# Kernel tuning notes

Hardware: AMD Instinct MI355X
Metric: run time of the kernel (lower is better)

## Reference

```python
import jax, jax.numpy as jnp
import numpy as np
import math

D_MODEL, D_STATE, SEQ_L = 1024, 64, 2048

def setup_inputs() -> dict:
    key = jax.random.key(0)
    k_dt, k_C = jax.random.split(key, 2)
    log_dt = jax.random.uniform(k_dt, (D_MODEL,), minval=math.log(0.001), maxval=math.log(0.1)).astype(jnp.float32)
    A_real = -0.5 * jnp.ones((D_MODEL, D_STATE), dtype=jnp.float32)
    A_imag = (jnp.repeat(jnp.arange(D_STATE, dtype=jnp.float32)[None, :], D_MODEL, axis=0) * math.pi)
    C = (jax.random.normal(k_C, (D_MODEL, D_STATE, 2)) * 0.5).astype(jnp.float32)
    return {"log_dt": log_dt, "A_real": A_real, "A_imag": A_imag, "C": C, "L": SEQ_L}

def reference(log_dt, A_real, A_imag, C, L):
    # dt: (D,1); A, C: (D,N) complex
    dt = jnp.exp(log_dt)[:, None]
    A = jax.lax.complex(A_real, A_imag)
    Cc = jax.lax.complex(C[..., 0], C[..., 1])
    dt_A = A * dt                                   # (D, N)
    A_bar = (1 + dt_A / 2) / (1 - dt_A / 2)         # (D, N) bilinear discretization
    B_bar = dt / (1 - dt_A / 2)                     # (D, N)
    z_inv = jnp.exp(-2j * jnp.pi * jnp.arange(L) / L)  # (L,) unit-circle frequencies
    # Cauchy-style broadcast-reduce: sum_n (C*B)_n / (1 - A_bar_n * z_inv_l)
    num = (Cc * B_bar)[:, :, None]                  # (D, N, 1)
    denom = 1 - A_bar[:, :, None] * z_inv[None, None, :]  # (D, N, L)
    H_z = jnp.sum(num / denom, axis=1)              # (D, L) complex transfer function
    return H_z
```

## Files before the change

kernel.cpp:

```cpp
#include <hip/hip_runtime.h>
#include <math.h>

constexpr int D_MODEL = 1024;
constexpr int D_STATE = 64;
constexpr int SEQ_L   = 2048;
constexpr int BLOCK   = 256;
constexpr int IPT     = 8;

__global__ __launch_bounds__(BLOCK) void s4_cauchy_real_kernel(
    const float* __restrict__ log_dt,
    const float* __restrict__ A_real,
    const float* __restrict__ A_imag,
    const float* __restrict__ C,
    float* __restrict__ out)
{
    __shared__ float s_abr[D_STATE];
    __shared__ float s_abi[D_STATE];
    __shared__ float s_nr [D_STATE];
    __shared__ float s_ni [D_STATE];

    const int d   = blockIdx.x;
    const int tid = threadIdx.x;

    if (tid < D_STATE) {
        const int n = tid;
        const float dt = __expf(log_dt[d]);
        const float ar = A_real[d * D_STATE + n];
        const float ai = A_imag[d * D_STATE + n];
        const float xr = 0.5f * dt * ar;
        const float xi = 0.5f * dt * ai;
        const float dr = 1.0f - xr;
        const float di = -xi;
        const float inv = 1.0f / (dr * dr + di * di);
        const float pr = 1.0f + xr;
        const float pi = xi;
        const float abr = (pr * dr + pi * di) * inv;
        const float abi = (pi * dr - pr * di) * inv;
        const float bbr =  dt * dr * inv;
        const float bbi = -dt * di * inv;
        const float cr = C[(d * D_STATE + n) * 2 + 0];
        const float ci = C[(d * D_STATE + n) * 2 + 1];
        s_abr[n] = abr;
        s_abi[n] = abi;
        s_nr[n]  = cr * bbr - ci * bbi;
        s_ni[n]  = cr * bbi + ci * bbr;
    }
    __syncthreads();

    float zr[IPT], zi[IPT], acc[IPT];
#pragma unroll
    for (int k = 0; k < IPT; ++k) {
        const int l = tid + k * BLOCK;
        const float theta = (2.0f * 3.14159265358979323846f * (float)l) / (float)SEQ_L;
        float s, c;
        __sincosf(theta, &s, &c);
        zr[k] = c;
        zi[k] = -s;
        acc[k] = 0.0f;
    }

#pragma unroll 4
    for (int n = 0; n < D_STATE; ++n) {
        const float abr = s_abr[n];
        const float abi = s_abi[n];
        const float nr  = s_nr[n];
        const float ni  = s_ni[n];
#pragma unroll
        for (int k = 0; k < IPT; ++k) {
            const float dr  = fmaf(-abr, zr[k], fmaf(abi, zi[k], 1.0f));
            const float di  = fmaf(-abr, zi[k], (-abi) * zr[k]);
            const float mag = fmaf(di, di, dr * dr);
            const float num = fmaf(ni, di, nr * dr);
            acc[k] = fmaf(num, __builtin_amdgcn_rcpf(mag), acc[k]);
        }
    }

#pragma unroll
    for (int k = 0; k < IPT; ++k)
        out[d * SEQ_L + tid + k * BLOCK] = acc[k];
}

__global__ __launch_bounds__(BLOCK) void s4_cauchy_complex_kernel(
    const float* __restrict__ log_dt, const float* __restrict__ A_real,
    const float* __restrict__ A_imag, const float* __restrict__ C,
    float* __restrict__ out)
{
    __shared__ float s_abr[D_STATE], s_abi[D_STATE], s_nr[D_STATE], s_ni[D_STATE];
    const int d    = blockIdx.x / (SEQ_L / BLOCK);
    const int lblk = blockIdx.x % (SEQ_L / BLOCK);
    const int tid  = threadIdx.x;
    if (tid < D_STATE) {
        const int n = tid;
        const float dt = __expf(log_dt[d]);
        const float ar = A_real[d * D_STATE + n], ai = A_imag[d * D_STATE + n];
        const float xr = 0.5f * dt * ar, xi = 0.5f * dt * ai;
        const float dr = 1.0f - xr, di = -xi;
        const float inv = 1.0f / (dr * dr + di * di);
        const float pr = 1.0f + xr, pi = xi;
        s_abr[n] = (pr * dr + pi * di) * inv;
        s_abi[n] = (pi * dr - pr * di) * inv;
        const float bbr = dt * dr * inv, bbi = -dt * di * inv;
        const float cr = C[(d * D_STATE + n) * 2 + 0], ci = C[(d * D_STATE + n) * 2 + 1];
        s_nr[n] = cr * bbr - ci * bbi;
        s_ni[n] = cr * bbi + ci * bbr;
    }
    __syncthreads();
    const int l = lblk * BLOCK + tid;
    const float theta = (2.0f * 3.14159265358979323846f * (float)l) / (float)SEQ_L;
    float s, c; __sincosf(theta, &s, &c);
    const float zr = c, zi = -s;
    float accr = 0.f, acci = 0.f;
#pragma unroll
    for (int n = 0; n < D_STATE; ++n) {
        const float abr = s_abr[n], abi = s_abi[n], nr = s_nr[n], ni = s_ni[n];
        const float dr = 1.0f - (abr * zr - abi * zi);
        const float di = -(abr * zi + abi * zr);
        const float inv = __builtin_amdgcn_rcpf(dr * dr + di * di);
        accr += (nr * dr + ni * di) * inv;
        acci += (ni * dr - nr * di) * inv;
    }
    float2* o = reinterpret_cast<float2*>(out);
    o[d * SEQ_L + l] = make_float2(accr, acci);
}

extern "C" void kernel_launch(void* const* d_in, const int* in_sizes, int n_in,
                              void* d_out, int out_size, void* d_ws, size_t ws_size,
                              hipStream_t stream) {
    const float* log_dt = (const float*)d_in[0];
    const float* A_real = (const float*)d_in[1];
    const float* A_imag = (const float*)d_in[2];
    const float* C      = (const float*)d_in[3];
    float* out = (float*)d_out;

    if (out_size >= 2 * D_MODEL * SEQ_L) {
        dim3 grid(D_MODEL * (SEQ_L / BLOCK));
        s4_cauchy_complex_kernel<<<grid, dim3(BLOCK), 0, stream>>>(log_dt, A_real, A_imag, C, out);
    } else {
        dim3 grid(D_MODEL);
        s4_cauchy_real_kernel<<<grid, dim3(BLOCK), 0, stream>>>(log_dt, A_real, A_imag, C, out);
    }
}
```

Measured before the change: 33.78 us.

## Pack real Cauchy kernel with f32x2 math, antipodal symmetry, and shared reciprocal

Rewrites the real-output kernel to use packed two-wide float vectors so the compiler can emit packed FMA instructions. It uses the z(l+L/2) = -z(l) symmetry to compute the A_bar*z product once for two output points. It also merges the two reciprocals into one rcp of the product of the two magnitudes. This cuts ALU and transcendental work per state element, at the cost of possible overflow or precision loss in mag1*mag2 and doubled shared-memory storage of broadcast coefficients.

```diff
diff --git a/kernel.cpp b/kernel.cpp
--- a/kernel.cpp
+++ b/kernel.cpp
@@ -5,7 +5,12 @@
 constexpr int D_STATE = 64;
 constexpr int SEQ_L   = 2048;
 constexpr int BLOCK   = 256;
-constexpr int IPT     = 8;
+
+typedef float f32x2 __attribute__((ext_vector_type(2)));
+
+static __device__ __forceinline__ f32x2 fma2(f32x2 a, f32x2 b, f32x2 c) {
+    return __builtin_elementwise_fma(a, b, c);
+}
 
 __global__ __launch_bounds__(BLOCK) void s4_cauchy_real_kernel(
     const float* __restrict__ log_dt,
@@ -14,10 +19,10 @@
     const float* __restrict__ C,
     float* __restrict__ out)
 {
-    __shared__ float s_abr[D_STATE];
-    __shared__ float s_abi[D_STATE];
-    __shared__ float s_nr [D_STATE];
-    __shared__ float s_ni [D_STATE];
+    __shared__ f32x2 s_ab_r[D_STATE];
+    __shared__ f32x2 s_ab_i[D_STATE];
+    __shared__ f32x2 s_n_r [D_STATE];
+    __shared__ f32x2 s_n_i [D_STATE];
 
     const int d   = blockIdx.x;
     const int tid = threadIdx.x;
@@ -40,44 +45,65 @@
         const float bbi = -dt * di * inv;
         const float cr = C[(d * D_STATE + n) * 2 + 0];
         const float ci = C[(d * D_STATE + n) * 2 + 1];
-        s_abr[n] = abr;
-        s_abi[n] = abi;
-        s_nr[n]  = cr * bbr - ci * bbi;
-        s_ni[n]  = cr * bbi + ci * bbr;
+        const float nr = cr * bbr - ci * bbi;
+        const float ni = cr * bbi + ci * bbr;
+        s_ab_r[n] = (f32x2){abr, abr};
+        s_ab_i[n] = (f32x2){abi, abi};
+        s_n_r [n] = (f32x2){nr, nr};
+        s_n_i [n] = (f32x2){ni, ni};
     }
     __syncthreads();
 
-    float zr[IPT], zi[IPT], acc[IPT];
+    f32x2 zr2[2], zi2[2], acc2[4];
 #pragma unroll
-    for (int k = 0; k < IPT; ++k) {
-        const int l = tid + k * BLOCK;
-        const float theta = (2.0f * 3.14159265358979323846f * (float)l) / (float)SEQ_L;
-        float s, c;
-        __sincosf(theta, &s, &c);
-        zr[k] = c;
-        zi[k] = -s;
-        acc[k] = 0.0f;
+    for (int kp = 0; kp < 2; ++kp) {
+#pragma unroll
+        for (int j = 0; j < 2; ++j) {
+            const int l = tid + (2 * kp + j) * BLOCK;
+            const float theta = (2.0f * 3.14159265358979323846f * (float)l) / (float)SEQ_L;
+            float s, c;
+            __sincosf(theta, &s, &c);
+            zr2[kp][j] = c;
+            zi2[kp][j] = -s;
+        }
+        acc2[kp]     = (f32x2){0.0f, 0.0f};
+        acc2[kp + 2] = (f32x2){0.0f, 0.0f};
     }
 
-#pragma unroll 4
+#pragma unroll 2
     for (int n = 0; n < D_STATE; ++n) {
-        const float abr = s_abr[n];
-        const float abi = s_abi[n];
-        const float nr  = s_nr[n];
-        const float ni  = s_ni[n];
+        const f32x2 ab_r = s_ab_r[n];
+        const f32x2 ab_i = s_ab_i[n];
+        const f32x2 n_r  = s_n_r[n];
+        const f32x2 n_i  = s_n_i[n];
 #pragma unroll
-        for (int k = 0; k < IPT; ++k) {
-            const float dr  = fmaf(-abr, zr[k], fmaf(abi, zi[k], 1.0f));
-            const float di  = fmaf(-abr, zi[k], (-abi) * zr[k]);
-            const float mag = fmaf(di, di, dr * dr);
-            const float num = fmaf(ni, di, nr * dr);
-            acc[k] = fmaf(num, __builtin_amdgcn_rcpf(mag), acc[k]);
+        for (int kp = 0; kp < 2; ++kp) {
+            const f32x2 ur = fma2(-ab_i, zi2[kp], ab_r * zr2[kp]);
+            const f32x2 ui = fma2( ab_i, zr2[kp], ab_r * zi2[kp]);
+            const f32x2 uisq = ui * ui;
+            const f32x2 dr1 = (f32x2){1.0f, 1.0f} - ur;
+            const f32x2 dr2 = (f32x2){1.0f, 1.0f} + ur;
+            const f32x2 mag1 = fma2(dr1, dr1, uisq);
+            const f32x2 mag2 = fma2(dr2, dr2, uisq);
+            const f32x2 num1 = fma2(-n_i, ui, n_r * dr1);
+            const f32x2 num2 = fma2( n_i, ui, n_r * dr2);
+            const f32x2 mm = mag1 * mag2;
+            f32x2 r;
+            r[0] = __builtin_amdgcn_rcpf(mm[0]);
+            r[1] = __builtin_amdgcn_rcpf(mm[1]);
+            acc2[kp]     = fma2(num1 * mag2, r, acc2[kp]);
+            acc2[kp + 2] = fma2(num2 * mag1, r, acc2[kp + 2]);
         }
     }
 
 #pragma unroll
-    for (int k = 0; k < IPT; ++k)
-        out[d * SEQ_L + tid + k * BLOCK] = acc[k];
+    for (int kp = 0; kp < 2; ++kp) {
+#pragma unroll
+        for (int j = 0; j < 2; ++j) {
+            out[d * SEQ_L + tid + (2 * kp + j) * BLOCK]        = acc2[kp][j];
+            out[d * SEQ_L + tid + (2 * kp + j + 4) * BLOCK]    = acc2[kp + 2][j];
+        }
+    }
 }
 
 __global__ __launch_bounds__(BLOCK) void s4_cauchy_complex_kernel(
```

Result: faster. 29.51 us (-12.6%).
